# Kernel tuning notes

Measured on AMD Instinct MI355X. Metric: run time of the kernel, lower is better.

Reference implementation:

```python
import jax, jax.numpy as jnp
import numpy as np

LORA_DIM = 16          # hard-coded in module
LORA_TOKEN_INDEX = 1   # lora_dim*layer_sequence + 1 with layer_sequence=0
B, S, D, H = 4, 2048, 1024, 4096  # num_hiddens = 4*num_input (forced by view())


def setup_inputs() -> dict:
    key = jax.random.key(0)
    ks = jax.random.split(key, 6)
    x = jax.random.normal(ks[0], (B, S, D), dtype=jnp.float32)
    W1 = jax.random.normal(ks[1], (H, D), dtype=jnp.float32) * 0.02
    b1 = jnp.zeros((H,), dtype=jnp.float32)
    W2 = jax.random.normal(ks[2], (D, H), dtype=jnp.float32) * 0.02
    b2 = jnp.zeros((D,), dtype=jnp.float32)
    scale = jnp.asarray(0.001, dtype=jnp.float32)  # nn.Parameter(torch.tensor(0.001))
    return {"x": x, "W1": W1, "b1": b1, "W2": W2, "b2": b2, "scale": scale}


def reference(x, W1, b1, W2, b2, scale):
    Bx, Sx, Dx = x.shape
    Hx = W1.shape[0]  # = 4*Dx
    # 16 lora tokens starting at LORA_TOKEN_INDEX
    lt = jax.lax.dynamic_slice_in_dim(x, LORA_TOKEN_INDEX, LORA_DIM, axis=1)
    even = lt[:, ::2, :]  # (B, 8, D)
    odd = lt[:, 1::2, :]  # (B, 8, D)
    # per-sample low-rank weight updates:
    # result_multiplication[b,k] = outer(even[b,k], odd[b,k]) (D,D)
    # matrix1 = first 4 blocks stacked -> (B, 4D, D); matrix2 = last 4 reshaped -> (B, D, 4D)
    m1 = (even[:, :4, :, None] * odd[:, :4, None, :]).reshape(Bx, Hx, Dx)
    m2 = (even[:, 4:, :, None] * odd[:, 4:, None, :]).reshape(Bx, Dx, Hx)
    # x @ (W1 + scale*m1)^T + b1, fused without repeating W1 per batch
    h = jnp.einsum('bsd,hd->bsh', x, W1) + scale * jnp.einsum('bsd,bhd->bsh', x, m1) + b1
    h = jax.nn.gelu(h, approximate=False)  # torch nn.GELU default = exact erf
    out = jnp.einsum('bsh,oh->bso', h, W2) + scale * jnp.einsum('bsh,boh->bso', h, m2) + b2
    return out
```

## Files before the change

### kernel.cpp

```cpp
#include <hip/hip_runtime.h>
#include <cstdint>
#include <cstddef>

#define MROWS 8192
#define DDIM  1024
#define HDIM  4096

typedef __bf16 bf16x8 __attribute__((ext_vector_type(8)));
typedef float  f32x4  __attribute__((ext_vector_type(4)));

typedef __attribute__((address_space(1))) void* as1_vp;
typedef __attribute__((address_space(3))) void* as3_vp;

__device__ __forceinline__ unsigned short f2bf(float f) {
  unsigned int u = __builtin_bit_cast(unsigned int, f);
  u += 0x7fffu + ((u >> 16) & 1u);
  return (unsigned short)(u >> 16);
}

__device__ __forceinline__ float fast_gelu(float x) {
  float x3 = x * x * x;
  float z = 0.7978845608028654f * x + 0.03567740814f * x3;
  float e = __builtin_amdgcn_exp2f(z * 2.8853900817779268f);
  float t = 1.0f - 2.0f * __builtin_amdgcn_rcpf(e + 1.0f);
  return 0.5f * x * (1.0f + t);
}

__device__ __forceinline__ void gld_lds16(const unsigned short* g, unsigned short* lds) {
  __builtin_amdgcn_global_load_lds((as1_vp)(uintptr_t)g, (as3_vp)lds, 16, 0, 0);
}

#define VMW(n)  asm volatile("s_waitcnt vmcnt(" #n ")" ::: "memory")
#define LKW()   asm volatile("s_waitcnt lgkmcnt(0)" ::: "memory")
#define BAR()   asm volatile("s_barrier" ::: "memory")

__global__ __launch_bounds__(256) void pre_kernel(
    const float* __restrict__ x, const float* __restrict__ w1,
    const float* __restrict__ w2, unsigned short* __restrict__ xb,
    unsigned short* __restrict__ w1b, unsigned short* __restrict__ w2b,
    float* __restrict__ p1) {
  if (blockIdx.x >= 2048) {
    const int j = blockIdx.x - 2048;
    const float4* src; ushort4* dst; int off0;
    if (j < 256) { src = (const float4*)w1; dst = (ushort4*)w1b; off0 = j * 4096 + threadIdx.x; }
    else         { src = (const float4*)w2; dst = (ushort4*)w2b; off0 = (j - 256) * 4096 + threadIdx.x; }
    float4 v[16];
#pragma unroll
    for (int k = 0; k < 16; ++k) v[k] = src[off0 + k * 256];
#pragma unroll
    for (int k = 0; k < 16; ++k) {
      ushort4 o;
      o.x = f2bf(v[k].x); o.y = f2bf(v[k].y); o.z = f2bf(v[k].z); o.w = f2bf(v[k].w);
      dst[off0 + k * 256] = o;
    }
    return;
  }
  const int bid = blockIdx.x;
  const int wave = threadIdx.x >> 6, lane = threadIdx.x & 63;
  const int m = bid * 4 + wave;
  const int b = m >> 11;
  const float4* xrow4 = (const float4*)(x + (size_t)m * DDIM);
  const float4* od4   = (const float4*)(x + ((size_t)b * 2048 + 2) * DDIM);
  ushort4* xbrow4 = (ushort4*)(xb + (size_t)m * DDIM);
  float a0 = 0.f, a1 = 0.f, a2 = 0.f, a3 = 0.f;
#pragma unroll
  for (int it = 0; it < 4; ++it) {
    int g = it * 64 + lane;
    float4 v = xrow4[g];
    ushort4 o; o.x = f2bf(v.x); o.y = f2bf(v.y); o.z = f2bf(v.z); o.w = f2bf(v.w);
    xbrow4[g] = o;
    float4 o0 = od4[g];
    float4 o1 = od4[512 + g];
    float4 o2 = od4[1024 + g];
    float4 o3 = od4[1536 + g];
    a0 += v.x * o0.x + v.y * o0.y + v.z * o0.z + v.w * o0.w;
    a1 += v.x * o1.x + v.y * o1.y + v.z * o1.z + v.w * o1.w;
    a2 += v.x * o2.x + v.y * o2.y + v.z * o2.z + v.w * o2.w;
    a3 += v.x * o3.x + v.y * o3.y + v.z * o3.z + v.w * o3.w;
  }
#pragma unroll
  for (int off = 32; off > 0; off >>= 1) {
    a0 += __shfl_down(a0, off);
    a1 += __shfl_down(a1, off);
    a2 += __shfl_down(a2, off);
    a3 += __shfl_down(a3, off);
  }
  if (lane == 0) {
    float4 r; r.x = a0; r.y = a1; r.z = a2; r.w = a3;
    ((float4*)p1)[m] = r;
  }
}

__global__ __launch_bounds__(512, 2) void gemm1_kernel(
    const unsigned short* __restrict__ xb, const unsigned short* __restrict__ w1b,
    const float* __restrict__ x, const float* __restrict__ b1,
    const float* __restrict__ p1, const float* __restrict__ scale_p,
    unsigned short* __restrict__ hact) {
  __shared__ __align__(16) unsigned short As[4 * 256 * 32];
  __shared__ __align__(16) unsigned short Bs[4 * 256 * 32];

  const int id = blockIdx.x;
  const int xcd = id & 7, w = id >> 3;
  const int m0 = (xcd * 4 + (w & 3)) * 256;
  const int n0 = (w >> 2) * 256;

  const int tid  = threadIdx.x;
  const int wave = tid >> 6, lane = tid & 63;
  const int quad = lane >> 4, l16 = lane & 15;
  const int wm2  = wave >> 2;
  const int wn2  = wave & 3;

  const unsigned short *gA0, *gA1, *gB0, *gB1;
  {
    int idx = tid;
    int r = idx >> 2, sl = idx & 3, c = (sl - (r >> 1)) & 3;
    gA0 = xb  + (size_t)(m0 + r) * DDIM + c * 8;
    gB0 = w1b + (size_t)(n0 + r) * DDIM + c * 8;
    idx = 512 + tid;
    r = idx >> 2; sl = idx & 3; c = (sl - (r >> 1)) & 3;
    gA1 = xb  + (size_t)(m0 + r) * DDIM + c * 8;
    gB1 = w1b + (size_t)(n0 + r) * DDIM + c * 8;
  }
  const int ldsOff0 = (wave * 64) * 8;
  const int ldsOff1 = (512 + wave * 64) * 8;

#define STAGE1(tt, sb) do {                                   \
    const int _k = (tt) * 32;                                 \
    unsigned short* _a = &As[(sb) * 8192];                    \
    unsigned short* _b = &Bs[(sb) * 8192];                    \
    gld_lds16(gA0 + _k, _a + ldsOff0);                        \
    gld_lds16(gA1 + _k, _a + ldsOff1);                        \
    gld_lds16(gB0 + _k, _b + ldsOff0);                        \
    gld_lds16(gB1 + _k, _b + ldsOff1);                        \
  } while (0)

  f32x4 acc[8][4];
  const f32x4 z = {0.f, 0.f, 0.f, 0.f};
#pragma unroll
  for (int i = 0; i < 8; ++i)
#pragma unroll
    for (int j = 0; j < 4; ++j) acc[i][j] = z;

  bf16x8 a[8], b[4];

  auto RA = [&](int nb) {
    const unsigned short* Ab = As + nb * 8192;
    const unsigned short* Bb = Bs + nb * 8192;
#pragma unroll
    for (int j = 0; j < 4; ++j) {
      const int rb = wn2 * 64 + j * 16 + l16;
      b[j] = *(const bf16x8*)(Bb + rb * 32 + ((quad + (rb >> 1)) & 3) * 8);
    }
#pragma unroll
    for (int i = 0; i < 4; ++i) {
      const int ra = wm2 * 128 + i * 16 + l16;
      a[i] = *(const bf16x8*)(Ab + ra * 32 + ((quad + (ra >> 1)) & 3) * 8);
    }
  };
  auto RB = [&](int cb) {
    const unsigned short* Ab = As + cb * 8192;
#pragma unroll
    for (int i = 4; i < 8; ++i) {
      const int ra = wm2 * 128 + i * 16 + l16;
      a[i] = *(const bf16x8*)(Ab + ra * 32 + ((quad + (ra >> 1)) & 3) * 8);
    }
  };
  auto MFA = [&]() {
    __builtin_amdgcn_s_setprio(1);
#pragma unroll
    for (int i = 0; i < 4; ++i)
#pragma unroll
      for (int j = 0; j < 4; ++j)
        acc[i][j] = __builtin_amdgcn_mfma_f32_16x16x32_bf16(a[i], b[j], acc[i][j], 0, 0, 0);
    __builtin_amdgcn_s_setprio(0);
  };
  auto MFB = [&]() {
    __builtin_amdgcn_s_setprio(1);
#pragma unroll
    for (int i = 4; i < 8; ++i)
#pragma unroll
      for (int j = 0; j < 4; ++j)
        acc[i][j] = __builtin_amdgcn_mfma_f32_16x16x32_bf16(a[i], b[j], acc[i][j], 0, 0, 0);
    __builtin_amdgcn_s_setprio(0);
  };

#define G1BODY(cb, sb, nb, tt) do {   \
    LKW(); MFA();                     \
    RB(cb);                           \
    STAGE1((tt) + 3, sb);             \
    VMW(8);                           \
    LKW(); MFB();                     \
    BAR();                            \
    RA(nb);                           \
  } while (0)

  STAGE1(0, 0);
  STAGE1(1, 1);
  STAGE1(2, 2);
  VMW(8); BAR();
  RA(0);

#pragma unroll 1
  for (int t = 0; t < 28; t += 4) {
    G1BODY(0, 3, 1, t + 0);
    G1BODY(1, 0, 2, t + 1);
    G1BODY(2, 1, 3, t + 2);
    G1BODY(3, 2, 0, t + 3);
  }
  LKW(); MFA(); RB(0); STAGE1(31, 3); VMW(8); LKW(); MFB(); BAR(); RA(1);
  LKW(); MFA(); RB(1); VMW(4); LKW(); MFB(); BAR(); RA(2);
  LKW(); MFA(); RB(2); VMW(0); LKW(); MFB(); BAR(); RA(3);
  LKW(); MFA(); RB(3); LKW(); MFB();

  const float sc = scale_p[0];
  const int bidx = m0 >> 11;
  const int i1 = (n0 + wn2 * 64) >> 10;
  const float* exrow = x + ((size_t)(bidx * 2048 + 1 + 2 * i1)) * DDIM;

  float exv[4], b1v[4]; int nn[4];
#pragma unroll
  for (int j = 0; j < 4; ++j) {
    nn[j]  = n0 + wn2 * 64 + j * 16 + l16;
    exv[j] = exrow[nn[j] & 1023];
    b1v[j] = b1[nn[j]];
  }
#pragma unroll
  for (int i = 0; i < 8; ++i) {
#pragma unroll
    for (int r = 0; r < 4; ++r) {
      const int m = m0 + wm2 * 128 + i * 16 + quad * 4 + r;
      const float pv = p1[(size_t)m * 4 + i1] * sc;
#pragma unroll
      for (int j = 0; j < 4; ++j) {
        float v = acc[i][j][r] + b1v[j] + pv * exv[j];
        hact[(size_t)m * HDIM + nn[j]] = f2bf(fast_gelu(v));
      }
    }
  }
#undef G1BODY
#undef STAGE1
}

__global__ __launch_bounds__(512, 2) void gemm2_kernel(
    const unsigned short* __restrict__ hact, const unsigned short* __restrict__ w2b,
    const float* __restrict__ x, const float* __restrict__ b2,
    const float* __restrict__ scale_p, float* __restrict__ out) {
  __shared__ __align__(16) unsigned short As[3 * 256 * 64];
  __shared__ __align__(16) unsigned short Bs[3 * 128 * 64];
  __shared__ __align__(16) unsigned short od_lds[1024];
  __shared__ __align__(16) float p2s[256 * 4];

  const int id = blockIdx.x;
  const int xcd = id & 7, w = id >> 3;
  const int m0 = (xcd * 4 + (w & 3)) * 256;
  const int n0 = (w >> 2) * 128;
  const int tid = threadIdx.x;
  const int wave = tid >> 6, lane = tid & 63, quad = lane >> 4, l16 = lane & 15;
  const int wmq = (wave >> 1) * 64;
  const int wnq = (wave & 1) * 64;
  const bool hi = (wave & 1);
  const int bidx = m0 >> 11;
  const int i2 = n0 >> 8;

  if (tid < 256) {
    const float4* src = (const float4*)(x + ((size_t)(bidx * 2048 + 10 + 2 * i2)) * DDIM);
    float4 v = src[tid];
    ushort4 o; o.x = f2bf(v.x); o.y = f2bf(v.y); o.z = f2bf(v.z); o.w = f2bf(v.w);
    ((ushort4*)od_lds)[tid] = o;
  }
  LKW();

  f32x4 acc[4][4];
  const f32x4 z = {0.f, 0.f, 0.f, 0.f};
#pragma unroll
  for (int i = 0; i < 4; ++i)
#pragma unroll
    for (int j = 0; j < 4; ++j) acc[i][j] = z;
  f32x4 pacc[2] = {z, z};
  const bf16x8 zer8 = __builtin_bit_cast(bf16x8, z);

  const unsigned short *gA[4], *gB[2];
#pragma unroll
  for (int s = 0; s < 4; ++s) {
    int idx = (wave * 4 + s) * 64 + lane;
    int r = idx >> 3, sl = idx & 7, c = (sl - r) & 7;
    gA[s] = hact + (size_t)(m0 + r) * HDIM + c * 8;
  }
#pragma unroll
  for (int s = 0; s < 2; ++s) {
    int idx = (wave * 2 + s) * 64 + lane;
    int r = idx >> 3, sl = idx & 7, c = (sl - r) & 7;
    gB[s] = w2b + (size_t)(n0 + r) * HDIM + c * 8;
  }

#define STAGE2(tt, sb) do {                                   \
    const int _k = (tt) * 64;                                 \
    unsigned short* _a = &As[(sb) * 16384];                   \
    unsigned short* _b = &Bs[(sb) * 8192];                    \
    gld_lds16(gA[0] + _k, _a + (wave * 4 + 0) * 512);         \
    gld_lds16(gA[1] + _k, _a + (wave * 4 + 1) * 512);         \
    gld_lds16(gA[2] + _k, _a + (wave * 4 + 2) * 512);         \
    gld_lds16(gA[3] + _k, _a + (wave * 4 + 3) * 512);         \
    gld_lds16(gB[0] + _k, _b + (wave * 2 + 0) * 512);         \
    gld_lds16(gB[1] + _k, _b + (wave * 2 + 1) * 512);         \
  } while (0)

  bf16x8 a[4], b[4], odv;

  auto RPH = [&](int nb, int kk, int odk) {
    const unsigned short* Ab = As + nb * 16384;
    const unsigned short* Bb = Bs + nb * 8192;
    odv = *(const bf16x8*)(od_lds + odk + kk + quad * 8);
    const int cb = (kk >> 3) + quad;
#pragma unroll
    for (int j = 0; j < 4; ++j) {
      const int rb = wnq + j * 16 + l16;
      b[j] = *(const bf16x8*)(Bb + rb * 64 + ((cb + rb) & 7) * 8);
    }
#pragma unroll
    for (int i = 0; i < 4; ++i) {
      const int ra = wmq + i * 16 + l16;
      a[i] = *(const bf16x8*)(Ab + ra * 64 + ((cb + ra) & 7) * 8);
    }
  };
  auto MPH = [&]() {
    bf16x8 bod = (l16 == 0) ? odv : zer8;
    bf16x8 pa0 = hi ? a[2] : a[0];
    bf16x8 pa1 = hi ? a[3] : a[1];
    pacc[0] = __builtin_amdgcn_mfma_f32_16x16x32_bf16(pa0, bod, pacc[0], 0, 0, 0);
    pacc[1] = __builtin_amdgcn_mfma_f32_16x16x32_bf16(pa1, bod, pacc[1], 0, 0, 0);
    __builtin_amdgcn_s_setprio(1);
#pragma unroll
    for (int i = 0; i < 4; ++i)
#pragma unroll
      for (int j = 0; j < 4; ++j)
        acc[i][j] = __builtin_amdgcn_mfma_f32_16x16x32_bf16(a[i], b[j], acc[i][j], 0, 0, 0);
    __builtin_amdgcn_s_setprio(0);
  };
  auto flush_p2 = [&](int seg) {
    const int ibase = hi ? 2 : 0;
    if (l16 == 0) {
#pragma unroll
      for (int ip = 0; ip < 2; ++ip)
#pragma unroll
        for (int e = 0; e < 4; ++e)
          p2s[(wmq + (ibase + ip) * 16 + quad * 4 + e) * 4 + seg] = pacc[ip][e];
    }
    pacc[0] = z; pacc[1] = z;
  };

#define G2BODY(tt, cb, sb, nb) do {                 \
    LKW(); MPH();                                   \
    RPH(cb, 32, ((tt) * 64) & 1023);                \
    STAGE2((tt) + 2, sb);                           \
    VMW(6);                                         \
    LKW(); MPH();                                   \
    if (((tt) & 15) == 15) flush_p2((tt) >> 4);     \
    BAR();                                          \
    RPH(nb, 0, (((tt) + 1) * 64) & 1023);           \
  } while (0)

  STAGE2(0, 0);
  STAGE2(1, 1);
  VMW(6); BAR();
  RPH(0, 0, 0);

#pragma unroll 1
  for (int t = 0; t < 60; t += 3) {
    G2BODY(t + 0, 0, 2, 1);
    G2BODY(t + 1, 1, 0, 2);
    G2BODY(t + 2, 2, 1, 0);
  }
  LKW(); MPH(); RPH(0, 32, (60 * 64) & 1023); STAGE2(62, 2); VMW(6);
  LKW(); MPH(); BAR(); RPH(1, 0, (61 * 64) & 1023);
  LKW(); MPH(); RPH(1, 32, (61 * 64) & 1023); STAGE2(63, 0); VMW(6);
  LKW(); MPH(); BAR(); RPH(2, 0, (62 * 64) & 1023);
  LKW(); MPH(); RPH(2, 32, (62 * 64) & 1023); VMW(0);
  LKW(); MPH(); BAR(); RPH(0, 0, (63 * 64) & 1023);
  LKW(); MPH(); RPH(0, 32, (63 * 64) & 1023);
  LKW(); MPH();
  flush_p2(3);
  LKW();
  BAR();

  const float sc = scale_p[0];
  const float* evrow = x + ((size_t)(bidx * 2048 + 9 + 2 * i2)) * DDIM;

  float4 ev[4]; float b2v[4]; int nn[4];
#pragma unroll
  for (int j = 0; j < 4; ++j) {
    nn[j] = n0 + wnq + j * 16 + l16;
    ev[j]  = *(const float4*)(evrow + 4 * (nn[j] & 255));
    b2v[j] = b2[nn[j]];
  }
#pragma unroll
  for (int i = 0; i < 4; ++i) {
#pragma unroll
    for (int r = 0; r < 4; ++r) {
      const int mloc = wmq + i * 16 + quad * 4 + r;
      const int m = m0 + mloc;
      const float4 pv = *(const float4*)(p2s + mloc * 4);
#pragma unroll
      for (int j = 0; j < 4; ++j) {
        float lora = ev[j].x * pv.x + ev[j].y * pv.y + ev[j].z * pv.z + ev[j].w * pv.w;
        out[(size_t)m * DDIM + nn[j]] = acc[i][j][r] + b2v[j] + sc * lora;
      }
    }
  }
#undef G2BODY
#undef STAGE2
}

extern "C" void kernel_launch(void* const* d_in, const int* in_sizes, int n_in,
                              void* d_out, int out_size, void* d_ws, size_t ws_size,
                              hipStream_t stream) {
  const float* x     = (const float*)d_in[0];
  const float* W1    = (const float*)d_in[1];
  const float* b1    = (const float*)d_in[2];
  const float* W2    = (const float*)d_in[3];
  const float* b2    = (const float*)d_in[4];
  const float* scale = (const float*)d_in[5];
  float* out = (float*)d_out;

  char* ws = (char*)d_ws;
  unsigned short* xb   = (unsigned short*)(ws);
  unsigned short* w1b  = (unsigned short*)(ws + 16777216);
  unsigned short* w2b  = (unsigned short*)(ws + 25165824);
  unsigned short* hact = (unsigned short*)(ws + 33554432);
  float*          p1   = (float*)(ws + 100663296);

  pre_kernel<<<dim3(2560), dim3(256), 0, stream>>>(x, W1, W2, xb, w1b, w2b, p1);
  gemm1_kernel<<<dim3(512), dim3(512), 0, stream>>>(xb, w1b, x, b1, p1, scale, hact);
  gemm2_kernel<<<dim3(256), dim3(512), 0, stream>>>(hact, w2b, x, b2, scale, out);
}
```

Baseline: 255.7 us.

## Load W1 fragments directly from global into registers in gemm1, dropping B LDS staging

```diff
diff --git a/kernel.cpp b/kernel.cpp
--- a/kernel.cpp
+++ b/kernel.cpp
@@ -91,13 +91,12 @@
   }
 }
 
-__global__ __launch_bounds__(512, 2) void gemm1_kernel(
+__global__ __launch_bounds__(512, 1) void gemm1_kernel(
     const unsigned short* __restrict__ xb, const unsigned short* __restrict__ w1b,
     const float* __restrict__ x, const float* __restrict__ b1,
     const float* __restrict__ p1, const float* __restrict__ scale_p,
     unsigned short* __restrict__ hact) {
-  __shared__ __align__(16) unsigned short As[4 * 256 * 32];
-  __shared__ __align__(16) unsigned short Bs[4 * 256 * 32];
+  __shared__ __align__(16) unsigned short As[4 * 8192];
 
   const int id = blockIdx.x;
   const int xcd = id & 7, w = id >> 3;
@@ -110,28 +109,35 @@
   const int wm2  = wave >> 2;
   const int wn2  = wave & 3;
 
-  const unsigned short *gA0, *gA1, *gB0, *gB1;
+  const unsigned short *gA0, *gA1;
   {
     int idx = tid;
     int r = idx >> 2, sl = idx & 3, c = (sl - (r >> 1)) & 3;
-    gA0 = xb  + (size_t)(m0 + r) * DDIM + c * 8;
-    gB0 = w1b + (size_t)(n0 + r) * DDIM + c * 8;
+    gA0 = xb + (size_t)(m0 + r) * DDIM + c * 8;
     idx = 512 + tid;
     r = idx >> 2; sl = idx & 3; c = (sl - (r >> 1)) & 3;
-    gA1 = xb  + (size_t)(m0 + r) * DDIM + c * 8;
-    gB1 = w1b + (size_t)(n0 + r) * DDIM + c * 8;
+    gA1 = xb + (size_t)(m0 + r) * DDIM + c * 8;
   }
   const int ldsOff0 = (wave * 64) * 8;
   const int ldsOff1 = (512 + wave * 64) * 8;
 
-#define STAGE1(tt, sb) do {                                   \
+#define STG_A(tt, sb) do {                                    \
     const int _k = (tt) * 32;                                 \
-    unsigned short* _a = &As[(sb) * 8192];                    \
-    unsigned short* _b = &Bs[(sb) * 8192];                    \
+    unsigned short* _a = As + (sb) * 8192;                    \
     gld_lds16(gA0 + _k, _a + ldsOff0);                        \
     gld_lds16(gA1 + _k, _a + ldsOff1);                        \
-    gld_lds16(gB0 + _k, _b + ldsOff0);                        \
-    gld_lds16(gB1 + _k, _b + ldsOff1);                        \
+  } while (0)
+
+  const unsigned short* gB[4];
+#pragma unroll
+  for (int j = 0; j < 4; ++j)
+    gB[j] = w1b + (size_t)(n0 + wn2 * 64 + j * 16 + l16) * DDIM + quad * 8;
+
+#define G_B(tt, bs) do {                                      \
+    bs[0] = *(const bf16x8*)(gB[0] + (tt) * 32);              \
+    bs[1] = *(const bf16x8*)(gB[1] + (tt) * 32);              \
+    bs[2] = *(const bf16x8*)(gB[2] + (tt) * 32);              \
+    bs[3] = *(const bf16x8*)(gB[3] + (tt) * 32);              \
   } while (0)
 
   f32x4 acc[8][4];
@@ -141,76 +147,88 @@
 #pragma unroll
     for (int j = 0; j < 4; ++j) acc[i][j] = z;
 
-  bf16x8 a[8], b[4];
-
-  auto RA = [&](int nb) {
+  bf16x8 a03A[4], a03B[4], a47[4];
+  bf16x8 bP[4], bQ[4];
+
+  auto RA03 = [&](int nb, bf16x8 (&aa)[4]) {
     const unsigned short* Ab = As + nb * 8192;
-    const unsigned short* Bb = Bs + nb * 8192;
-#pragma unroll
-    for (int j = 0; j < 4; ++j) {
-      const int rb = wn2 * 64 + j * 16 + l16;
-      b[j] = *(const bf16x8*)(Bb + rb * 32 + ((quad + (rb >> 1)) & 3) * 8);
-    }
 #pragma unroll
     for (int i = 0; i < 4; ++i) {
       const int ra = wm2 * 128 + i * 16 + l16;
-      a[i] = *(const bf16x8*)(Ab + ra * 32 + ((quad + (ra >> 1)) & 3) * 8);
-    }
-  };
-  auto RB = [&](int cb) {
+      aa[i] = *(const bf16x8*)(Ab + ra * 32 + ((quad + (ra >> 1)) & 3) * 8);
+    }
+  };
+  auto RB47 = [&](int cb) {
     const unsigned short* Ab = As + cb * 8192;
 #pragma unroll
-    for (int i = 4; i < 8; ++i) {
-      const int ra = wm2 * 128 + i * 16 + l16;
-      a[i] = *(const bf16x8*)(Ab + ra * 32 + ((quad + (ra >> 1)) & 3) * 8);
-    }
-  };
-  auto MFA = [&]() {
+    for (int i = 0; i < 4; ++i) {
+      const int ra = wm2 * 128 + (i + 4) * 16 + l16;
+      a47[i] = *(const bf16x8*)(Ab + ra * 32 + ((quad + (ra >> 1)) & 3) * 8);
+    }
+  };
+  auto MFA = [&](bf16x8 (&aa)[4], bf16x8 (&bs)[4]) {
     __builtin_amdgcn_s_setprio(1);
 #pragma unroll
     for (int i = 0; i < 4; ++i)
 #pragma unroll
       for (int j = 0; j < 4; ++j)
-        acc[i][j] = __builtin_amdgcn_mfma_f32_16x16x32_bf16(a[i], b[j], acc[i][j], 0, 0, 0);
+        acc[i][j] = __builtin_amdgcn_mfma_f32_16x16x32_bf16(aa[i], bs[j], acc[i][j], 0, 0, 0);
     __builtin_amdgcn_s_setprio(0);
   };
-  auto MFB = [&]() {
+  auto MFB = [&](bf16x8 (&bs)[4]) {
     __builtin_amdgcn_s_setprio(1);
 #pragma unroll
-    for (int i = 4; i < 8; ++i)
+    for (int i = 0; i < 4; ++i)
 #pragma unroll
       for (int j = 0; j < 4; ++j)
-        acc[i][j] = __builtin_amdgcn_mfma_f32_16x16x32_bf16(a[i], b[j], acc[i][j], 0, 0, 0);
+        acc[4 + i][j] = __builtin_amdgcn_mfma_f32_16x16x32_bf16(a47[i], bs[j], acc[4 + i][j], 0, 0, 0);
     __builtin_amdgcn_s_setprio(0);
   };
 
-#define G1BODY(cb, sb, nb, tt) do {   \
-    LKW(); MFA();                     \
-    RB(cb);                           \
-    STAGE1((tt) + 3, sb);             \
-    VMW(8);                           \
-    LKW(); MFB();                     \
-    BAR();                            \
-    RA(nb);                           \
+#define BODY(tt, CB, SB, NB, ACUR, ANXT, BCUR, BNXT) do {     \
+    VMW(2);                                                   \
+    LKW(); MFA(a03##ACUR, BCUR);                              \
+    RB47(CB);                                                 \
+    G_B((tt) + 1, BNXT);                                      \
+    STG_A((tt) + 3, SB);                                      \
+    LKW(); MFB(BCUR);                                         \
+    BAR();                                                    \
+    RA03(NB, a03##ANXT);                                      \
   } while (0)
 
-  STAGE1(0, 0);
-  STAGE1(1, 1);
-  STAGE1(2, 2);
-  VMW(8); BAR();
-  RA(0);
+  STG_A(0, 0);
+  STG_A(1, 1);
+  G_B(0, bP);
+  VMW(4); BAR();
+  RA03(0, a03A);
+  STG_A(2, 2);
 
 #pragma unroll 1
   for (int t = 0; t < 28; t += 4) {
-    G1BODY(0, 3, 1, t + 0);
-    G1BODY(1, 0, 2, t + 1);
-    G1BODY(2, 1, 3, t + 2);
-    G1BODY(3, 2, 0, t + 3);
-  }
-  LKW(); MFA(); RB(0); STAGE1(31, 3); VMW(8); LKW(); MFB(); BAR(); RA(1);
-  LKW(); MFA(); RB(1); VMW(4); LKW(); MFB(); BAR(); RA(2);
-  LKW(); MFA(); RB(2); VMW(0); LKW(); MFB(); BAR(); RA(3);
-  LKW(); MFA(); RB(3); LKW(); MFB();
+    BODY(t + 0, 0, 3, 1, A, B, bP, bQ);
+    BODY(t + 1, 1, 0, 2, B, A, bQ, bP);
+    BODY(t + 2, 2, 1, 3, A, B, bP, bQ);
+    BODY(t + 3, 3, 2, 0, B, A, bQ, bP);
+  }
+  BODY(28, 0, 3, 1, A, B, bP, bQ);
+  VMW(2);
+  LKW(); MFA(a03B, bQ);
+  RB47(1);
+  G_B(30, bP);
+  LKW(); MFB(bQ);
+  BAR();
+  RA03(2, a03A);
+  VMW(0);
+  LKW(); MFA(a03A, bP);
+  RB47(2);
+  G_B(31, bQ);
+  LKW(); MFB(bP);
+  BAR();
+  RA03(3, a03B);
+  VMW(0);
+  LKW(); MFA(a03B, bQ);
+  RB47(3);
+  LKW(); MFB(bQ);
 
   const float sc = scale_p[0];
   const int bidx = m0 >> 11;
@@ -237,8 +255,9 @@
       }
     }
   }
-#undef G1BODY
-#undef STAGE1
+#undef BODY
+#undef STG_A
+#undef G_B
 }
 
 __global__ __launch_bounds__(512, 2) void gemm2_kernel(
```

New measurement: 269.6 us. +5.4%, slower.
